# Optimization experiments

Hardware: AMD Instinct MI355X
Metric: run time of the kernel (lower is better)

The kernel has to match this reference:

```python
import jax, jax.numpy as jnp
import numpy as np

B, N, DIM, HEADS, DEPTH, MLP = 4, 1024, 256, 4, 4, 1024
DH = DIM // HEADS
EPS = 1e-5


def _ln(x, g, b):
    mu = jnp.mean(x, axis=-1, keepdims=True)
    var = jnp.mean((x - mu) ** 2, axis=-1, keepdims=True)
    return (x - mu) / jnp.sqrt(var + EPS) * g + b


def setup_inputs() -> dict:
    key = jax.random.key(0)
    ks = jax.random.split(key, 10)
    s = 0.02
    p = {}
    p["x"] = jax.random.normal(ks[0], (B, N, DIM), jnp.float32)
    p["attn_bias"] = jax.random.normal(ks[1], (2, B, HEADS, N, N), jnp.float32)
    p["ln1_g"] = jnp.ones((DEPTH, DIM), jnp.float32)
    p["ln1_b"] = jnp.zeros((DEPTH, DIM), jnp.float32)
    p["Wkv"] = jax.random.normal(ks[2], (DEPTH, DIM, 2 * DIM), jnp.float32) * s
    p["Wq"] = jax.random.normal(ks[3], (DEPTH, DIM, DIM), jnp.float32) * s
    p["Wo"] = jax.random.normal(ks[4], (DEPTH, DIM, DIM), jnp.float32) * s
    p["bo"] = jnp.zeros((DEPTH, DIM), jnp.float32)
    p["ln2_g"] = jnp.ones((DEPTH, DIM), jnp.float32)
    p["ln2_b"] = jnp.zeros((DEPTH, DIM), jnp.float32)
    p["W1"] = jax.random.normal(ks[5], (DEPTH, DIM, MLP), jnp.float32) * s
    p["b1"] = jnp.zeros((DEPTH, MLP), jnp.float32)
    p["W2"] = jax.random.normal(ks[6], (DEPTH, MLP, DIM), jnp.float32) * s
    p["b2"] = jnp.zeros((DEPTH, DIM), jnp.float32)
    p["Wg"] = jax.random.normal(ks[7], (DIM, DIM), jnp.float32) * s
    p["lng_g"] = jnp.ones((DIM,), jnp.float32)
    p["lng_b"] = jnp.zeros((DIM,), jnp.float32)
    return p


def reference(x, attn_bias, ln1_g, ln1_b, Wkv, Wq, Wo, bo, ln2_g, ln2_b, W1, b1, W2, b2, Wg, lng_g, lng_b):
    scale = DIM ** -0.5
    add_attn = attn_bias[0] + attn_bias[1]            # [B,H,N,N]
    # aggregation bias matrices are layer-invariant (recomputed identically each layer in torch)
    A = jnp.mean(attn_bias[0], axis=1)                # [B,N,N]
    S = jnp.mean(attn_bias[1], axis=1)
    G = jax.nn.softmax(A * S, axis=2)                 # [B,N,N]

    def split_heads(t):  # [B,N,DIM] -> [B,H,N,DH]
        return t.reshape(B, N, HEADS, DH).transpose(0, 2, 1, 3)

    for l in range(DEPTH):
        # softmax-GCN aggregation
        x_ma = jax.nn.relu(_ln(jnp.matmul(G, x) @ Wg, lng_g, lng_b))
        # attention (PreNorm on x only; q comes from un-normed x_ma)
        xn = _ln(x, ln1_g[l], ln1_b[l])
        kv = xn @ Wkv[l]
        k, v = jnp.split(kv, 2, axis=-1)
        q = x_ma @ Wq[l]
        qh, kh, vh = split_heads(q), split_heads(k), split_heads(v)
        dots = jnp.einsum('bhid,bhjd->bhij', qh, kh) * scale + add_attn
        attn = jax.nn.softmax(dots, axis=-1)
        out = jnp.einsum('bhij,bhjd->bhid', attn, vh)
        out = out.transpose(0, 2, 1, 3).reshape(B, N, DIM)
        x = x + out @ Wo[l] + bo[l]
        # feed-forward (exact GELU, matching torch nn.GELU default)
        xn2 = _ln(x, ln2_g[l], ln2_b[l])
        x = x + jax.nn.gelu(xn2 @ W1[l] + b1[l], approximate=False) @ W2[l] + b2[l]
    return x
```

## Files before the change

kernel.cpp:

```cpp
#include <hip/hip_runtime.h>
#include <hip/hip_bf16.h>
#include <math.h>

typedef unsigned short u16;
typedef __bf16 bf16x8 __attribute__((ext_vector_type(8)));
typedef float f32x4 __attribute__((ext_vector_type(4)));

#define B_ 4
#define N_ 1024
#define DIM_ 256
#define HEADS_ 4
#define DH_ 64
#define MLP_ 1024
#define DEPTH_ 4

__device__ __forceinline__ float r2f(u16 r){ return __uint_as_float(((unsigned)r)<<16); }
__device__ __forceinline__ u16 f2r(float f){ __hip_bfloat16 h = __float2bfloat16(f); return *(u16*)&h; }

__device__ __forceinline__ float gelu_exact(float v){
  return 0.5f*v*(1.0f + erff(v*0.70710678118654752440f));
}

#define MFMA16(a,b,c) __builtin_amdgcn_mfma_f32_16x16x32_bf16(a,b,c,0,0,0)

__global__ void prep_bias(const float* __restrict__ bias, u16* __restrict__ G, u16* __restrict__ bsum){
  int blk = blockIdx.x;
  int i = blk & (N_-1);
  int b = blk >> 10;
  int t = threadIdx.x;
  __shared__ float sc[N_];
  __shared__ float red[256];
  long long base0 = ((long long)(b*HEADS_)*N_ + i)*(long long)N_;
  const long long hs = (long long)N_*N_;
  const long long cs = (long long)B_*HEADS_*N_*N_;
  float lmax = -3e38f;
  for (int jj=0;jj<4;jj++){
    int j = t + jj*256;
    float a = 0.f, s = 0.f;
    #pragma unroll
    for (int h=0;h<HEADS_;h++){
      float x0 = bias[base0 + h*hs + j];
      float x1 = bias[cs + base0 + h*hs + j];
      a += x0; s += x1;
      bsum[base0 + h*hs + j] = f2r(x0 + x1);
    }
    float v = (a*0.25f)*(s*0.25f);
    sc[j] = v;
    lmax = fmaxf(lmax, v);
  }
  red[t]=lmax; __syncthreads();
  for (int s=128;s>0;s>>=1){ if(t<s) red[t]=fmaxf(red[t],red[t+s]); __syncthreads(); }
  float m = red[0]; __syncthreads();
  float lsum = 0.f;
  for (int jj=0;jj<4;jj++){
    int j = t + jj*256;
    float e = __expf(sc[j]-m);
    sc[j]=e; lsum+=e;
  }
  red[t]=lsum; __syncthreads();
  for (int s=128;s>0;s>>=1){ if(t<s) red[t]+=red[t+s]; __syncthreads(); }
  float inv = 1.0f/red[0];
  u16* Grow = G + ((long long)b*N_ + i)*(long long)N_;
  for (int jj=0;jj<4;jj++){ int j=t+jj*256; Grow[j]=f2r(sc[j]*inv); }
}

__global__ void ln_kernel(const float* __restrict__ X, u16* __restrict__ Y,
                          const float* __restrict__ g, const float* __restrict__ bvec){
  int row = blockIdx.x, t = threadIdx.x;
  __shared__ float red[256];
  float v = X[(long long)row*DIM_ + t];
  red[t]=v; __syncthreads();
  for (int s=128;s>0;s>>=1){ if(t<s) red[t]+=red[t+s]; __syncthreads(); }
  float mu = red[0]*(1.0f/DIM_); __syncthreads();
  float d = v - mu;
  red[t]=d*d; __syncthreads();
  for (int s=128;s>0;s>>=1){ if(t<s) red[t]+=red[t+s]; __syncthreads(); }
  float var = red[0]*(1.0f/DIM_);
  Y[(long long)row*DIM_ + t] = f2r(d*rsqrtf(var+1e-5f)*g[t] + bvec[t]);
}

__global__ void tcast_all(const float* __restrict__ Wkv, const float* __restrict__ Wq,
                          const float* __restrict__ Wo, const float* __restrict__ W1,
                          const float* __restrict__ W2, const float* __restrict__ Wg,
                          const float* __restrict__ xin,
                          u16* WkvT, u16* WqT, u16* WoT, u16* W1T, u16* W2T, u16* WgT, u16* xT){
  int z = blockIdx.z;
  const float* I; u16* O; int ldin, R, C;
  if (z < 4)       { I = Wkv + z*131072;      O = WkvT + z*131072;      ldin=512;  R=256;  C=512;  }
  else if (z < 8)  { I = Wq  + (z-4)*65536;   O = WqT  + (z-4)*65536;   ldin=256;  R=256;  C=256;  }
  else if (z < 12) { I = Wo  + (z-8)*65536;   O = WoT  + (z-8)*65536;   ldin=256;  R=256;  C=256;  }
  else if (z < 16) { I = W1  + (z-12)*262144; O = W1T  + (z-12)*262144; ldin=1024; R=256;  C=1024; }
  else if (z < 20) { I = W2  + (z-16)*262144; O = W2T  + (z-16)*262144; ldin=256;  R=1024; C=256;  }
  else if (z == 20){ I = Wg;                  O = WgT;                  ldin=256;  R=256;  C=256;  }
  else             { I = xin + (z-21)*262144; O = xT   + (z-21)*262144; ldin=256;  R=1024; C=256;  }
  int c0 = blockIdx.x*32, r0 = blockIdx.y*32;
  if (c0 >= C || r0 >= R) return;
  __shared__ float tile[32][33];
  int tx = threadIdx.x, ty = threadIdx.y;
  #pragma unroll
  for (int i=0;i<4;i++)
    tile[ty*4+i][tx] = I[(long long)(r0+ty*4+i)*ldin + c0+tx];
  __syncthreads();
  #pragma unroll
  for (int i=0;i<4;i++)
    O[(long long)(c0+ty*4+i)*R + r0+tx] = f2r(tile[tx][ty*4+i]);
}

__global__ __launch_bounds__(512) void layer_pre(
    const u16* __restrict__ Gb, const u16* __restrict__ xT, const u16* __restrict__ xnb,
    const u16* __restrict__ WgT, const u16* __restrict__ WqT, const u16* __restrict__ WkvT,
    const float* __restrict__ lng, const float* __restrict__ lnb,
    u16* __restrict__ qb, u16* __restrict__ kvb, u16* __restrict__ vt)
{
  __shared__ float Gx_s[16][264];
  __shared__ float t2_s[16][264];
  __shared__ u16  xma_s[16][264];
  int tid = threadIdx.x;
  int w = tid>>6, lane = tid&63, lr = lane&15, qd = lane>>4;
  int row0 = blockIdx.x*16;
  int batch = row0>>10, brow0 = row0&1023;

  {
    int kw = w>>2, cw = w&3;
    const u16* Ap = Gb + (long long)batch*1048576 + (long long)(brow0+lr)*1024 + kw*512;
    const u16* Bp = xT + (long long)batch*262144 + (long long)kw*512;
    f32x4 acc[4] = {};
    for (int k0=0;k0<512;k0+=32){
      bf16x8 af = *(const bf16x8*)(Ap + k0 + qd*8);
      #pragma unroll
      for (int nt=0;nt<4;nt++){
        bf16x8 bf = *(const bf16x8*)(Bp + (long long)(cw*64+nt*16+lr)*1024 + k0 + qd*8);
        acc[nt] = MFMA16(af,bf,acc[nt]);
      }
    }
    if (kw==0){
      #pragma unroll
      for (int nt=0;nt<4;nt++)
        #pragma unroll
        for (int r=0;r<4;r++) Gx_s[qd*4+r][cw*64+nt*16+lr] = acc[nt][r];
    }
    __syncthreads();
    if (kw==1){
      #pragma unroll
      for (int nt=0;nt<4;nt++)
        #pragma unroll
        for (int r=0;r<4;r++) Gx_s[qd*4+r][cw*64+nt*16+lr] += acc[nt][r];
    }
    __syncthreads();
  }
  {
    f32x4 acc[2] = {};
    for (int k0=0;k0<256;k0+=32){
      bf16x8 af;
      #pragma unroll
      for (int i=0;i<8;i++) af[i] = (__bf16)Gx_s[lr][k0+qd*8+i];
      #pragma unroll
      for (int i=0;i<2;i++){
        bf16x8 bf = *(const bf16x8*)(WgT + (long long)((w*2+i)*16+lr)*256 + k0 + qd*8);
        acc[i] = MFMA16(af,bf,acc[i]);
      }
    }
    #pragma unroll
    for (int i=0;i<2;i++)
      #pragma unroll
      for (int r=0;r<4;r++) t2_s[qd*4+r][(w*2+i)*16+lr] = acc[i][r];
  }
  __syncthreads();
  {
    int r = tid>>5, cg = tid&31;
    float v[8]; float s=0.f;
    #pragma unroll
    for (int i=0;i<8;i++){ v[i] = t2_s[r][cg*8+i]; s += v[i]; }
    s += __shfl_xor(s,1); s += __shfl_xor(s,2); s += __shfl_xor(s,4); s += __shfl_xor(s,8); s += __shfl_xor(s,16);
    float mu = s*(1.0f/256.0f);
    float s2=0.f;
    #pragma unroll
    for (int i=0;i<8;i++){ float d=v[i]-mu; s2 += d*d; }
    s2 += __shfl_xor(s2,1); s2 += __shfl_xor(s2,2); s2 += __shfl_xor(s2,4); s2 += __shfl_xor(s2,8); s2 += __shfl_xor(s2,16);
    float rstd = rsqrtf(s2*(1.0f/256.0f)+1e-5f);
    #pragma unroll
    for (int i=0;i<8;i++){
      int c = cg*8+i;
      float y = (v[i]-mu)*rstd*lng[c] + lnb[c];
      xma_s[r][c] = f2r(fmaxf(y,0.f));
    }
  }
  __syncthreads();
  {
    f32x4 acc[2] = {};
    for (int k0=0;k0<256;k0+=32){
      bf16x8 af = *(const bf16x8*)&xma_s[lr][k0+qd*8];
      #pragma unroll
      for (int i=0;i<2;i++){
        bf16x8 bf = *(const bf16x8*)(WqT + (long long)((w*2+i)*16+lr)*256 + k0 + qd*8);
        acc[i] = MFMA16(af,bf,acc[i]);
      }
    }
    #pragma unroll
    for (int i=0;i<2;i++)
      #pragma unroll
      for (int r=0;r<4;r++)
        qb[(long long)(row0+qd*4+r)*DIM_ + (w*2+i)*16+lr] = f2r(acc[i][r]);
  }
  {
    const u16* Ap = xnb + (long long)(row0+lr)*DIM_;
    f32x4 acc[4] = {};
    for (int k0=0;k0<256;k0+=32){
      bf16x8 af = *(const bf16x8*)(Ap + k0 + qd*8);
      #pragma unroll
      for (int i=0;i<4;i++){
        bf16x8 bf = *(const bf16x8*)(WkvT + (long long)((w*4+i)*16+lr)*256 + k0 + qd*8);
        acc[i] = MFMA16(af,bf,acc[i]);
      }
    }
    #pragma unroll
    for (int i=0;i<4;i++){
      int col = (w*4+i)*16+lr;
      #pragma unroll
      for (int r=0;r<4;r++){
        int row = row0+qd*4+r;
        float v = acc[i][r];
        kvb[(long long)row*512 + col] = f2r(v);
        if (col >= 256)
          vt[(long long)batch*262144 + (long long)(col-256)*1024 + (row&1023)] = f2r(v);
      }
    }
  }
}

__global__ __launch_bounds__(256) void flash_attn(
    const u16* __restrict__ qb, const u16* __restrict__ kvb,
    const u16* __restrict__ vt, const u16* __restrict__ bsum,
    u16* __restrict__ out)
{
  int z = blockIdx.z;
  int b = z>>2, h = z&3;
  int qt = blockIdx.x;
  int tid = threadIdx.x;
  int w = tid>>6, lane = tid&63;
  int lr = lane&15, qd = lane>>4;
  __shared__ u16 Pl[4][16][72];
  __shared__ u16 sb[4][16][72];

  int qrow0 = qt*64 + w*16;
  const u16* qp = qb + ((long long)(b*N_) + qrow0 + lr)*DIM_ + h*DH_;
  bf16x8 aq0 = *(const bf16x8*)(qp + qd*8);
  bf16x8 aq1 = *(const bf16x8*)(qp + 32 + qd*8);

  f32x4 oacc[4] = {};
  float m_r[4] = {-3e38f,-3e38f,-3e38f,-3e38f};
  float l_r[4] = {0.f,0.f,0.f,0.f};

  const u16* kbase = kvb + ((long long)(b*N_))*512 + h*DH_;
  const u16* vbase = vt + (long long)b*(DIM_*N_) + (long long)(h*DH_)*N_;
  const u16* bias_base = bsum + ((long long)z*N_ + qrow0)*(long long)N_;
  int srr = lane>>2, scc = (lane&3)*16;

  for (int jt=0; jt<16; jt++){
    int j0 = jt*64;
    {
      const u16* gs = bias_base + (long long)srr*N_ + j0 + scc;
      uint4 t0 = *(const uint4*)gs;
      uint4 t1 = *(const uint4*)(gs+8);
      *(uint4*)&sb[w][srr][scc]   = t0;
      *(uint4*)&sb[w][srr][scc+8] = t1;
    }
    f32x4 sacc[4] = {};
    #pragma unroll
    for (int nt=0; nt<4; nt++){
      const u16* kp = kbase + (long long)(j0 + nt*16 + lr)*512;
      bf16x8 bk0 = *(const bf16x8*)(kp + qd*8);
      bf16x8 bk1 = *(const bf16x8*)(kp + 32 + qd*8);
      sacc[nt] = MFMA16(aq0, bk0, sacc[nt]);
      sacc[nt] = MFMA16(aq1, bk1, sacc[nt]);
    }
    #pragma unroll
    for (int r=0;r<4;r++){
      float pv[4];
      float vmax = -3e38f;
      #pragma unroll
      for (int nt=0;nt<4;nt++){
        float v = sacc[nt][r]*0.0625f + r2f(sb[w][qd*4+r][nt*16+lr]);
        pv[nt] = v;
        vmax = fmaxf(vmax, v);
      }
      vmax = fmaxf(vmax, __shfl_xor(vmax,1));
      vmax = fmaxf(vmax, __shfl_xor(vmax,2));
      vmax = fmaxf(vmax, __shfl_xor(vmax,4));
      vmax = fmaxf(vmax, __shfl_xor(vmax,8));
      float newm = fmaxf(m_r[r], vmax);
      float alpha = __expf(m_r[r]-newm);
      m_r[r] = newm;
      float psum = 0.f;
      #pragma unroll
      for (int nt=0;nt<4;nt++){
        float p = __expf(pv[nt]-newm);
        psum += p;
        Pl[w][qd*4+r][nt*16+lr] = f2r(p);
      }
      psum += __shfl_xor(psum,1);
      psum += __shfl_xor(psum,2);
      psum += __shfl_xor(psum,4);
      psum += __shfl_xor(psum,8);
      l_r[r] = l_r[r]*alpha + psum;
      #pragma unroll
      for (int ot=0;ot<4;ot++) oacc[ot][r] *= alpha;
    }
    #pragma unroll
    for (int ks=0;ks<2;ks++){
      bf16x8 ap = *(const bf16x8*)&Pl[w][lr][ks*32 + qd*8];
      #pragma unroll
      for (int ot=0;ot<4;ot++){
        const u16* vp = vbase + (long long)(ot*16+lr)*N_ + j0 + ks*32 + qd*8;
        bf16x8 bv = *(const bf16x8*)vp;
        oacc[ot] = MFMA16(ap, bv, oacc[ot]);
      }
    }
  }
  #pragma unroll
  for (int r=0;r<4;r++){
    float inv = 1.0f/l_r[r];
    #pragma unroll
    for (int ot=0;ot<4;ot++){
      out[((long long)(b*N_) + qrow0 + qd*4 + r)*DIM_ + h*DH_ + ot*16 + lr]
          = f2r(oacc[ot][r]*inv);
    }
  }
}

__global__ __launch_bounds__(512) void layer_post(
    const u16* __restrict__ aob, const float* __restrict__ resx,
    const u16* __restrict__ WoT, const float* __restrict__ bo,
    const float* __restrict__ ln2g, const float* __restrict__ ln2b,
    const u16* __restrict__ W1T, const float* __restrict__ b1,
    const u16* __restrict__ W2T, const float* __restrict__ b2,
    float* __restrict__ xf_out,
    const float* __restrict__ ln1g_next, const float* __restrict__ ln1b_next,
    u16* __restrict__ xn_out, u16* __restrict__ xT_out)
{
  __shared__ float v_s[16][264];
  __shared__ u16  xn2_s[16][264];
  __shared__ u16  h1_s[16][1048];
  __shared__ float xnew_s[16][264];
  int tid = threadIdx.x;
  int w = tid>>6, lane = tid&63, lr = lane&15, qd = lane>>4;
  int row0 = blockIdx.x*16;
  int batch = row0>>10;

  {
    const u16* Ap = aob + (long long)(row0+lr)*DIM_;
    f32x4 acc[2] = {};
    for (int k0=0;k0<256;k0+=32){
      bf16x8 af = *(const bf16x8*)(Ap + k0 + qd*8);
      #pragma unroll
      for (int i=0;i<2;i++){
        bf16x8 bf = *(const bf16x8*)(WoT + (long long)((w*2+i)*16+lr)*256 + k0 + qd*8);
        acc[i] = MFMA16(af,bf,acc[i]);
      }
    }
    #pragma unroll
    for (int i=0;i<2;i++){
      int col = (w*2+i)*16+lr;
      #pragma unroll
      for (int r=0;r<4;r++)
        v_s[qd*4+r][col] = acc[i][r] + bo[col] + resx[(long long)(row0+qd*4+r)*DIM_ + col];
    }
  }
  __syncthreads();
  {
    int r = tid>>5, cg = tid&31;
    float v[8]; float s=0.f;
    #pragma unroll
    for (int i=0;i<8;i++){ v[i] = v_s[r][cg*8+i]; s += v[i]; }
    s += __shfl_xor(s,1); s += __shfl_xor(s,2); s += __shfl_xor(s,4); s += __shfl_xor(s,8); s += __shfl_xor(s,16);
    float mu = s*(1.0f/256.0f);
    float s2=0.f;
    #pragma unroll
    for (int i=0;i<8;i++){ float d=v[i]-mu; s2 += d*d; }
    s2 += __shfl_xor(s2,1); s2 += __shfl_xor(s2,2); s2 += __shfl_xor(s2,4); s2 += __shfl_xor(s2,8); s2 += __shfl_xor(s2,16);
    float rstd = rsqrtf(s2*(1.0f/256.0f)+1e-5f);
    #pragma unroll
    for (int i=0;i<8;i++){
      int c = cg*8+i;
      xn2_s[r][c] = f2r((v[i]-mu)*rstd*ln2g[c] + ln2b[c]);
    }
  }
  __syncthreads();
  {
    f32x4 acc[8] = {};
    for (int k0=0;k0<256;k0+=32){
      bf16x8 af = *(const bf16x8*)&xn2_s[lr][k0+qd*8];
      #pragma unroll
      for (int i=0;i<8;i++){
        bf16x8 bf = *(const bf16x8*)(W1T + (long long)((w*8+i)*16+lr)*256 + k0 + qd*8);
        acc[i] = MFMA16(af,bf,acc[i]);
      }
    }
    #pragma unroll
    for (int i=0;i<8;i++){
      int col = (w*8+i)*16+lr;
      #pragma unroll
      for (int r=0;r<4;r++)
        h1_s[qd*4+r][col] = f2r(gelu_exact(acc[i][r] + b1[col]));
    }
  }
  __syncthreads();
  {
    f32x4 acc[2] = {};
    for (int k0=0;k0<1024;k0+=32){
      bf16x8 af = *(const bf16x8*)&h1_s[lr][k0+qd*8];
      #pragma unroll
      for (int i=0;i<2;i++){
        bf16x8 bf = *(const bf16x8*)(W2T + (long long)((w*2+i)*16+lr)*1024 + k0 + qd*8);
        acc[i] = MFMA16(af,bf,acc[i]);
      }
    }
    #pragma unroll
    for (int i=0;i<2;i++){
      int col = (w*2+i)*16+lr;
      #pragma unroll
      for (int r=0;r<4;r++){
        float v = acc[i][r] + b2[col] + v_s[qd*4+r][col];
        xf_out[(long long)(row0+qd*4+r)*DIM_ + col] = v;
        xnew_s[qd*4+r][col] = v;
      }
    }
  }
  if (ln1g_next){
    __syncthreads();
    int r = tid>>5, cg = tid&31;
    float v[8]; float s=0.f;
    #pragma unroll
    for (int i=0;i<8;i++){ v[i] = xnew_s[r][cg*8+i]; s += v[i]; }
    s += __shfl_xor(s,1); s += __shfl_xor(s,2); s += __shfl_xor(s,4); s += __shfl_xor(s,8); s += __shfl_xor(s,16);
    float mu = s*(1.0f/256.0f);
    float s2=0.f;
    #pragma unroll
    for (int i=0;i<8;i++){ float d=v[i]-mu; s2 += d*d; }
    s2 += __shfl_xor(s2,1); s2 += __shfl_xor(s2,2); s2 += __shfl_xor(s2,4); s2 += __shfl_xor(s2,8); s2 += __shfl_xor(s2,16);
    float rstd = rsqrtf(s2*(1.0f/256.0f)+1e-5f);
    int grow = row0 + r;
    #pragma unroll
    for (int i=0;i<8;i++){
      int c = cg*8+i;
      xn_out[(long long)grow*DIM_ + c] = f2r((v[i]-mu)*rstd*ln1g_next[c] + ln1b_next[c]);
      xT_out[(long long)batch*262144 + (long long)c*1024 + (grow&1023)] = f2r(v[i]);
    }
  }
}

extern "C" void kernel_launch(void* const* d_in, const int* in_sizes, int n_in,
                              void* d_out, int out_size, void* d_ws, size_t ws_size,
                              hipStream_t stream){
  const float* x_in   = (const float*)d_in[0];
  const float* abias  = (const float*)d_in[1];
  const float* ln1_g  = (const float*)d_in[2];
  const float* ln1_b  = (const float*)d_in[3];
  const float* Wkv    = (const float*)d_in[4];
  const float* Wq     = (const float*)d_in[5];
  const float* Wo     = (const float*)d_in[6];
  const float* bo     = (const float*)d_in[7];
  const float* ln2_g  = (const float*)d_in[8];
  const float* ln2_b  = (const float*)d_in[9];
  const float* W1     = (const float*)d_in[10];
  const float* b1     = (const float*)d_in[11];
  const float* W2     = (const float*)d_in[12];
  const float* b2     = (const float*)d_in[13];
  const float* Wg     = (const float*)d_in[14];
  const float* lng_g  = (const float*)d_in[15];
  const float* lng_b  = (const float*)d_in[16];

  char* ws = (char*)d_ws;
  float* xf   = (float*)(ws);
  u16*  Gb    = (u16*)(ws + (4ll<<20));
  u16*  bsum  = (u16*)(ws + (12ll<<20));
  u16*  kvb   = (u16*)(ws + (44ll<<20));
  u16*  vt    = (u16*)(ws + (48ll<<20));
  u16*  xT    = (u16*)(ws + (50ll<<20));
  u16*  xnb   = (u16*)(ws + (52ll<<20));
  u16*  qb    = (u16*)(ws + (54ll<<20));
  u16*  aob   = (u16*)(ws + (56ll<<20));
  u16*  WkvT  = (u16*)(ws + (58ll<<20));
  u16*  WqT   = (u16*)(ws + (59ll<<20));
  u16*  WoT   = (u16*)(ws + (59ll<<20) + (512ll<<10));
  u16*  W1T   = (u16*)(ws + (60ll<<20));
  u16*  W2T   = (u16*)(ws + (62ll<<20));
  u16*  WgT   = (u16*)(ws + (64ll<<20));

  dim3 b256(256), b512(512);

  prep_bias<<<dim3(B_*N_), b256, 0, stream>>>(abias, Gb, bsum);
  tcast_all<<<dim3(32,32,25), dim3(32,8), 0, stream>>>(Wkv,Wq,Wo,W1,W2,Wg,x_in,
                                                       WkvT,WqT,WoT,W1T,W2T,WgT,xT);
  ln_kernel<<<dim3(B_*N_), b256, 0, stream>>>(x_in, xnb, ln1_g, ln1_b);

  for (int l=0; l<DEPTH_; l++){
    const float* resx = (l==0) ? x_in : xf;
    layer_pre<<<dim3(256), b512, 0, stream>>>(Gb, xT, xnb,
        WgT, WqT + (long long)l*65536, WkvT + (long long)l*131072,
        lng_g, lng_b, qb, kvb, vt);
    flash_attn<<<dim3(16,1,B_*HEADS_), b256, 0, stream>>>(qb, kvb, vt, bsum, aob);
    if (l < DEPTH_-1){
      layer_post<<<dim3(256), b512, 0, stream>>>(aob, resx,
          WoT + (long long)l*65536, bo + l*DIM_, ln2_g + l*DIM_, ln2_b + l*DIM_,
          W1T + (long long)l*262144, b1 + l*MLP_, W2T + (long long)l*262144, b2 + l*DIM_,
          xf, ln1_g + (l+1)*DIM_, ln1_b + (l+1)*DIM_, xnb, xT);
    } else {
      layer_post<<<dim3(256), b512, 0, stream>>>(aob, resx,
          WoT + (long long)l*65536, bo + l*DIM_, ln2_g + l*DIM_, ln2_b + l*DIM_,
          W1T + (long long)l*262144, b1 + l*MLP_, W2T + (long long)l*262144, b2 + l*DIM_,
          (float*)d_out, nullptr, nullptr, nullptr, nullptr);
    }
  }
}
```

Measured before the change: 727.2 us.

## Split KV across wave groups in flash attention and vectorise prep/LN kernels

Flash attention now runs 8 waves per block, with two groups each processing half of the key tiles for the same 64 query rows. The partial outputs, maxima and sums are merged through shared memory. This raises occupancy on an undersubscribed grid, at the cost of extra LDS and a merge step. prep_bias and ln_kernel are also rewritten with vector loads, register-held values and warp-shuffle reductions, and layer_pre converts Gx to bf16 once in shared memory before the Wg MFMA loop.

```diff
diff --git a/kernel.cpp b/kernel.cpp
--- a/kernel.cpp
+++ b/kernel.cpp
@@ -28,55 +28,70 @@
   int i = blk & (N_-1);
   int b = blk >> 10;
   int t = threadIdx.x;
-  __shared__ float sc[N_];
   __shared__ float red[256];
   long long base0 = ((long long)(b*HEADS_)*N_ + i)*(long long)N_;
   const long long hs = (long long)N_*N_;
   const long long cs = (long long)B_*HEADS_*N_*N_;
-  float lmax = -3e38f;
-  for (int jj=0;jj<4;jj++){
-    int j = t + jj*256;
-    float a = 0.f, s = 0.f;
-    #pragma unroll
-    for (int h=0;h<HEADS_;h++){
-      float x0 = bias[base0 + h*hs + j];
-      float x1 = bias[cs + base0 + h*hs + j];
-      a += x0; s += x1;
-      bsum[base0 + h*hs + j] = f2r(x0 + x1);
-    }
-    float v = (a*0.25f)*(s*0.25f);
-    sc[j] = v;
-    lmax = fmaxf(lmax, v);
-  }
+  int j0 = t*4;
+  f32x4 a = {0.f,0.f,0.f,0.f}, s = {0.f,0.f,0.f,0.f};
+  #pragma unroll
+  for (int h=0;h<HEADS_;h++){
+    f32x4 x0 = *(const f32x4*)(bias + base0 + h*hs + j0);
+    f32x4 x1 = *(const f32x4*)(bias + cs + base0 + h*hs + j0);
+    a += x0; s += x1;
+    union { ushort4 u; u16 e[4]; } pk;
+    #pragma unroll
+    for (int k=0;k<4;k++) pk.e[k] = f2r(x0[k]+x1[k]);
+    *(ushort4*)(bsum + base0 + h*hs + j0) = pk.u;
+  }
+  float v[4]; float lmax = -3e38f;
+  #pragma unroll
+  for (int k=0;k<4;k++){ v[k] = (a[k]*0.25f)*(s[k]*0.25f); lmax = fmaxf(lmax, v[k]); }
   red[t]=lmax; __syncthreads();
-  for (int s=128;s>0;s>>=1){ if(t<s) red[t]=fmaxf(red[t],red[t+s]); __syncthreads(); }
+  for (int st=128;st>0;st>>=1){ if(t<st) red[t]=fmaxf(red[t],red[t+st]); __syncthreads(); }
   float m = red[0]; __syncthreads();
-  float lsum = 0.f;
-  for (int jj=0;jj<4;jj++){
-    int j = t + jj*256;
-    float e = __expf(sc[j]-m);
-    sc[j]=e; lsum+=e;
-  }
+  float e[4]; float lsum = 0.f;
+  #pragma unroll
+  for (int k=0;k<4;k++){ e[k] = __expf(v[k]-m); lsum += e[k]; }
   red[t]=lsum; __syncthreads();
-  for (int s=128;s>0;s>>=1){ if(t<s) red[t]+=red[t+s]; __syncthreads(); }
+  for (int st=128;st>0;st>>=1){ if(t<st) red[t]+=red[t+st]; __syncthreads(); }
   float inv = 1.0f/red[0];
   u16* Grow = G + ((long long)b*N_ + i)*(long long)N_;
-  for (int jj=0;jj<4;jj++){ int j=t+jj*256; Grow[j]=f2r(sc[j]*inv); }
+  union { ushort4 u; u16 e[4]; } pg;
+  #pragma unroll
+  for (int k=0;k<4;k++) pg.e[k] = f2r(e[k]*inv);
+  *(ushort4*)(Grow + j0) = pg.u;
 }
 
 __global__ void ln_kernel(const float* __restrict__ X, u16* __restrict__ Y,
                           const float* __restrict__ g, const float* __restrict__ bvec){
-  int row = blockIdx.x, t = threadIdx.x;
-  __shared__ float red[256];
-  float v = X[(long long)row*DIM_ + t];
-  red[t]=v; __syncthreads();
-  for (int s=128;s>0;s>>=1){ if(t<s) red[t]+=red[t+s]; __syncthreads(); }
-  float mu = red[0]*(1.0f/DIM_); __syncthreads();
-  float d = v - mu;
-  red[t]=d*d; __syncthreads();
-  for (int s=128;s>0;s>>=1){ if(t<s) red[t]+=red[t+s]; __syncthreads(); }
-  float var = red[0]*(1.0f/DIM_);
-  Y[(long long)row*DIM_ + t] = f2r(d*rsqrtf(var+1e-5f)*g[t] + bvec[t]);
+  int row = blockIdx.x*8 + (threadIdx.x>>5);
+  int cg = threadIdx.x&31;
+  const float* xp = X + (long long)row*DIM_ + cg*8;
+  f32x4 v0 = *(const f32x4*)xp;
+  f32x4 v1 = *(const f32x4*)(xp+4);
+  float s = v0[0]+v0[1]+v0[2]+v0[3]+v1[0]+v1[1]+v1[2]+v1[3];
+  s += __shfl_xor(s,1); s += __shfl_xor(s,2); s += __shfl_xor(s,4); s += __shfl_xor(s,8); s += __shfl_xor(s,16);
+  float mu = s*(1.0f/256.0f);
+  float s2 = 0.f;
+  #pragma unroll
+  for (int k=0;k<4;k++){ float d=v0[k]-mu; s2 += d*d; }
+  #pragma unroll
+  for (int k=0;k<4;k++){ float d=v1[k]-mu; s2 += d*d; }
+  s2 += __shfl_xor(s2,1); s2 += __shfl_xor(s2,2); s2 += __shfl_xor(s2,4); s2 += __shfl_xor(s2,8); s2 += __shfl_xor(s2,16);
+  float rstd = rsqrtf(s2*(1.0f/256.0f)+1e-5f);
+  f32x4 g0 = *(const f32x4*)(g + cg*8);
+  f32x4 g1 = *(const f32x4*)(g + cg*8 + 4);
+  f32x4 b0 = *(const f32x4*)(bvec + cg*8);
+  f32x4 b1 = *(const f32x4*)(bvec + cg*8 + 4);
+  union { ushort4 u[2]; u16 e[8]; } pk;
+  #pragma unroll
+  for (int k=0;k<4;k++) pk.e[k]   = f2r((v0[k]-mu)*rstd*g0[k] + b0[k]);
+  #pragma unroll
+  for (int k=0;k<4;k++) pk.e[4+k] = f2r((v1[k]-mu)*rstd*g1[k] + b1[k]);
+  u16* yp = Y + (long long)row*DIM_ + cg*8;
+  *(ushort4*)yp = pk.u[0];
+  *(ushort4*)(yp+4) = pk.u[1];
 }
 
 __global__ void tcast_all(const float* __restrict__ Wkv, const float* __restrict__ Wq,
@@ -149,11 +164,15 @@
     __syncthreads();
   }
   {
+    int r = tid>>5, cg = tid&31;
+    #pragma unroll
+    for (int i=0;i<8;i++) xma_s[r][cg*8+i] = f2r(Gx_s[r][cg*8+i]);
+  }
+  __syncthreads();
+  {
     f32x4 acc[2] = {};
     for (int k0=0;k0<256;k0+=32){
-      bf16x8 af;
-      #pragma unroll
-      for (int i=0;i<8;i++) af[i] = (__bf16)Gx_s[lr][k0+qd*8+i];
+      bf16x8 af = *(const bf16x8*)&xma_s[lr][k0+qd*8];
       #pragma unroll
       for (int i=0;i<2;i++){
         bf16x8 bf = *(const bf16x8*)(WgT + (long long)((w*2+i)*16+lr)*256 + k0 + qd*8);
@@ -228,7 +247,7 @@
   }
 }
 
-__global__ __launch_bounds__(256) void flash_attn(
+__global__ __launch_bounds__(512) void flash_attn(
     const u16* __restrict__ qb, const u16* __restrict__ kvb,
     const u16* __restrict__ vt, const u16* __restrict__ bsum,
     u16* __restrict__ out)
@@ -238,11 +257,15 @@
   int qt = blockIdx.x;
   int tid = threadIdx.x;
   int w = tid>>6, lane = tid&63;
+  int g = w>>2, tw = w&3;
   int lr = lane&15, qd = lane>>4;
-  __shared__ u16 Pl[4][16][72];
-  __shared__ u16 sb[4][16][72];
-
-  int qrow0 = qt*64 + w*16;
+  __shared__ u16 Pl[8][16][72];
+  __shared__ u16 sb[8][16][72];
+  __shared__ float Ol[8][16][68];
+  __shared__ float Ml[8][16];
+  __shared__ float Ll[8][16];
+
+  int qrow0 = qt*64 + tw*16;
   const u16* qp = qb + ((long long)(b*N_) + qrow0 + lr)*DIM_ + h*DH_;
   bf16x8 aq0 = *(const bf16x8*)(qp + qd*8);
   bf16x8 aq1 = *(const bf16x8*)(qp + 32 + qd*8);
@@ -256,8 +279,8 @@
   const u16* bias_base = bsum + ((long long)z*N_ + qrow0)*(long long)N_;
   int srr = lane>>2, scc = (lane&3)*16;
 
-  for (int jt=0; jt<16; jt++){
-    int j0 = jt*64;
+  for (int jtl=0; jtl<8; jtl++){
+    int j0 = (g*8 + jtl)*64;
     {
       const u16* gs = bias_base + (long long)srr*N_ + j0 + scc;
       uint4 t0 = *(const uint4*)gs;
@@ -319,11 +342,25 @@
   }
   #pragma unroll
   for (int r=0;r<4;r++){
-    float inv = 1.0f/l_r[r];
-    #pragma unroll
-    for (int ot=0;ot<4;ot++){
-      out[((long long)(b*N_) + qrow0 + qd*4 + r)*DIM_ + h*DH_ + ot*16 + lr]
-          = f2r(oacc[ot][r]*inv);
+    int row = qd*4+r;
+    #pragma unroll
+    for (int ot=0;ot<4;ot++) Ol[w][row][ot*16+lr] = oacc[ot][r];
+    if (lr==0){ Ml[w][row] = m_r[r]; Ll[w][row] = l_r[r]; }
+  }
+  __syncthreads();
+  if (w < 4){
+    #pragma unroll
+    for (int r=0;r<4;r++){
+      int row = qd*4+r;
+      float m0 = Ml[w][row], m1 = Ml[w+4][row];
+      float mm = fmaxf(m0,m1);
+      float e0 = __expf(m0-mm), e1 = __expf(m1-mm);
+      float inv = 1.0f/(Ll[w][row]*e0 + Ll[w+4][row]*e1);
+      #pragma unroll
+      for (int ot=0;ot<4;ot++){
+        float o = Ol[w][row][ot*16+lr]*e0 + Ol[w+4][row][ot*16+lr]*e1;
+        out[((long long)(b*N_) + qrow0 + row)*DIM_ + h*DH_ + ot*16 + lr] = f2r(o*inv);
+      }
     }
   }
 }
@@ -492,14 +529,14 @@
   prep_bias<<<dim3(B_*N_), b256, 0, stream>>>(abias, Gb, bsum);
   tcast_all<<<dim3(32,32,25), dim3(32,8), 0, stream>>>(Wkv,Wq,Wo,W1,W2,Wg,x_in,
                                                        WkvT,WqT,WoT,W1T,W2T,WgT,xT);
-  ln_kernel<<<dim3(B_*N_), b256, 0, stream>>>(x_in, xnb, ln1_g, ln1_b);
+  ln_kernel<<<dim3(512), b256, 0, stream>>>(x_in, xnb, ln1_g, ln1_b);
 
   for (int l=0; l<DEPTH_; l++){
     const float* resx = (l==0) ? x_in : xf;
     layer_pre<<<dim3(256), b512, 0, stream>>>(Gb, xT, xnb,
         WgT, WqT + (long long)l*65536, WkvT + (long long)l*131072,
         lng_g, lng_b, qb, kvb, vt);
-    flash_attn<<<dim3(16,1,B_*HEADS_), b256, 0, stream>>>(qb, kvb, vt, bsum, aob);
+    flash_attn<<<dim3(16,1,B_*HEADS_), b512, 0, stream>>>(qb, kvb, vt, bsum, aob);
     if (l < DEPTH_-1){
       layer_post<<<dim3(256), b512, 0, stream>>>(aob, resx,
           WoT + (long long)l*65536, bo + l*DIM_, ln2_g + l*DIM_, ln2_b + l*DIM_,
```

New measurement: 760.9 us. 1.05x slower.
